# Performance work log

Measured on AMD Instinct MI355X. Metric: run time of the kernel, lower is better.

Reference implementation:

```python
import jax, jax.numpy as jnp
import numpy as np

NUM_PROTOTYPES = 512
NUM_BLOCKS = 8
D_MODEL = 1024
D_BLOCK = D_MODEL // NUM_BLOCKS


def setup_inputs() -> dict:
    key = jax.random.key(0)
    kq, km = jax.random.split(key)
    queries = jax.random.normal(kq, (8, 1024, D_MODEL), dtype=jnp.float32)
    # learned codebook: nn.Embedding(num_blocks*num_prototypes, d_block), normal init
    mem = jax.random.normal(km, (NUM_BLOCKS * NUM_PROTOTYPES, D_BLOCK), dtype=jnp.float32)
    return {"queries": queries, "mem": mem}


def reference(queries, mem):
    B, N, _ = queries.shape
    m, p, d = NUM_BLOCKS, NUM_PROTOTYPES, D_BLOCK
    q = queries.reshape(B, N, m, d)                 # [B,N,m,d]
    codes = mem.reshape(m, p, d)                    # [m,p,d]
    # Squared distances restricted to each query's own block (the only entries
    # the original consumes via distances[i, :, i]):
    #   ||q||^2 - 2 q.c + ||c||^2
    dots = jnp.einsum('bnmd,mpd->bnmp', q, codes)   # [B,N,m,p]
    qn = jnp.sum(q * q, axis=-1)                    # [B,N,m]
    cn = jnp.sum(codes * codes, axis=-1)            # [m,p]
    dist = qn[..., None] - 2.0 * dots + cn[None, None]
    local = jnp.argmin(dist, axis=-1)               # [B,N,m], first-min tiebreak like torch max of -dist
    indices = local + jnp.arange(m, dtype=local.dtype)[None, None, :] * p
    emb = codes[jnp.arange(m)[None, None, :], local]          # [B,N,m,d]
    emb = emb.reshape(B, N, m * d)
    # straight-through estimator
    emb_st = jax.lax.stop_gradient(emb - queries) + queries
    vq_loss = jnp.asarray(0.0, dtype=queries.dtype)
    commitment_loss = jnp.mean((jax.lax.stop_gradient(emb) - queries) ** 2)
    return emb_st, indices, vq_loss, commitment_loss
```

## Files before the change

kernel.cpp:

```cpp
#include <hip/hip_runtime.h>

#define NPROTO 512
#define NBLK 8
#define DB 128
#define DM 1024

#define IDX_OFF  8388608
#define VQ_OFF   8454144
#define CL_OFF   8454145

typedef unsigned short u16;
typedef __attribute__((ext_vector_type(8))) _Float16 f16x8;
typedef __attribute__((ext_vector_type(16))) float f32x16;

#define BH_B   0u
#define BL_B   1048576u
#define CN_B   2097152u
#define PART_B 2113536u
#define WS_NEED (PART_B + 8192u)

__global__ __launch_bounds__(256) void vq_prep(const float* __restrict__ src,
                                               u16* __restrict__ hi,
                                               u16* __restrict__ lo,
                                               float* __restrict__ cn) {
    const int t  = threadIdx.x;
    const int p  = blockIdx.x * 32 + (t >> 3);
    const int g  = t & 7;
    const int m  = p >> 9, pm = p & 511;
    const float* s = src + (size_t)p * DB + g * 16;
    float sq = 0.f;
    ushort4 h[4], l[4];
    #pragma unroll
    for (int j = 0; j < 4; ++j) {
        float4 v = *(const float4*)(s + j * 4);
        float x; _Float16 hf;
        #define S1(c, f) x = v.c; hf = (_Float16)x; h[j].f = __builtin_bit_cast(u16, hf); \
            hf = (_Float16)(x - (float)hf); l[j].f = __builtin_bit_cast(u16, hf); sq += x * x;
        S1(x, x) S1(y, y) S1(z, z) S1(w, w)
        #undef S1
    }
    const size_t o0 = ((size_t)((m * 8 + g) * 2 + 0) * 512 + pm) * 8;
    const size_t o1 = ((size_t)((m * 8 + g) * 2 + 1) * 512 + pm) * 8;
    *(uint4*)(hi + o0) = *(uint4*)&h[0];
    *(uint4*)(hi + o1) = *(uint4*)&h[2];
    *(uint4*)(lo + o0) = *(uint4*)&l[0];
    *(uint4*)(lo + o1) = *(uint4*)&l[2];
    sq += __shfl_xor(sq, 1, 64);
    sq += __shfl_xor(sq, 2, 64);
    sq += __shfl_xor(sq, 4, 64);
    if ((t & 7) == 0) cn[p] = sq;
}

__device__ __forceinline__ unsigned cvt2(float x, float y, unsigned& lo) {
    _Float16 hx = (_Float16)x, hy = (_Float16)y;
    _Float16 lx = (_Float16)(x - (float)hx), ly = (_Float16)(y - (float)hy);
    lo = (unsigned)__builtin_bit_cast(u16, lx) | ((unsigned)__builtin_bit_cast(u16, ly) << 16);
    return (unsigned)__builtin_bit_cast(u16, hx) | ((unsigned)__builtin_bit_cast(u16, hy) << 16);
}

__global__ __launch_bounds__(256, 2) void vq_fused(
        const float* __restrict__ q, const float* __restrict__ mem,
        const u16* __restrict__ bh, const u16* __restrict__ bl,
        const float* __restrict__ cn, float* __restrict__ out,
        float* __restrict__ partials) {
    __shared__ __align__(16) char smem0[16896];
    __shared__ u16  sidxv[4][32][33];
    __shared__ float finalv[4][32];
    __shared__ int   finali[4][32];
    __shared__ float qn_lds[32];
    __shared__ int   bp[32];
    __shared__ float lossbuf[32];

    u16   (*Ap)[8][66][8] = (u16 (*)[8][66][8])smem0;
    float (*sval)[32][33] = (float (*)[32][33])smem0;

    const int t    = threadIdx.x;
    const int lane = t & 63;
    const int w    = t >> 6;
    const int col  = lane & 31;
    const int kg   = lane >> 5;
    const int m    = blockIdx.y;
    const int bn0  = blockIdx.x * 32;

    {
        const int row = t >> 3, g = t & 7;
        const float* src = q + (size_t)(bn0 + row) * DM + m * DB + g * 16;
        float4 v0 = ((const float4*)src)[0];
        float4 v1 = ((const float4*)src)[1];
        float4 v2 = ((const float4*)src)[2];
        float4 v3 = ((const float4*)src)[3];
        float sq = v0.x*v0.x+v0.y*v0.y+v0.z*v0.z+v0.w*v0.w
                 + v1.x*v1.x+v1.y*v1.y+v1.z*v1.z+v1.w*v1.w
                 + v2.x*v2.x+v2.y*v2.y+v2.z*v2.z+v2.w*v2.w
                 + v3.x*v3.x+v3.y*v3.y+v3.z*v3.z+v3.w*v3.w;
        unsigned l0,l1,l2,l3,l4,l5,l6,l7;
        unsigned h0 = cvt2(v0.x, v0.y, l0), h1 = cvt2(v0.z, v0.w, l1);
        unsigned h2 = cvt2(v1.x, v1.y, l2), h3 = cvt2(v1.z, v1.w, l3);
        unsigned h4 = cvt2(v2.x, v2.y, l4), h5 = cvt2(v2.z, v2.w, l5);
        unsigned h6 = cvt2(v3.x, v3.y, l6), h7 = cvt2(v3.z, v3.w, l7);
        *(uint4*)&Ap[0][g][row][0]      = make_uint4(h0, h1, h2, h3);
        *(uint4*)&Ap[0][g][row + 32][0] = make_uint4(h4, h5, h6, h7);
        *(uint4*)&Ap[1][g][row][0]      = make_uint4(l0, l1, l2, l3);
        *(uint4*)&Ap[1][g][row + 32][0] = make_uint4(l4, l5, l6, l7);
        sq += __shfl_xor(sq, 1, 64);
        sq += __shfl_xor(sq, 2, 64);
        sq += __shfl_xor(sq, 4, 64);
        if (g == 0) qn_lds[row] = sq;
    }
    __syncthreads();

    const int pbase = w * 128;
    const u16* bh_l = bh + ((size_t)(m * 16 + kg) * 512 + pbase + col) * 8;
    const u16* bl_l = bl + ((size_t)(m * 16 + kg) * 512 + pbase + col) * 8;

    float bestv[16]; int besti[16];
    #pragma unroll
    for (int r = 0; r < 16; ++r) { bestv[r] = 3.4e38f; besti[r] = 0; }

    #pragma unroll 2
    for (int c = 0; c < 4; ++c) {
        const float cnv = cn[m * NPROTO + pbase + c * 32 + col];
        const u16* bhc = bh_l + c * 256;
        const u16* blc = bl_l + c * 256;
        f32x16 aA, aB;
        #pragma unroll
        for (int r = 0; r < 16; ++r) { aA[r] = 0.f; aB[r] = 0.f; }
        #pragma unroll
        for (int kst = 0; kst < 8; ++kst) {
            f16x8 Bh = *(const f16x8*)(bhc + kst * 8192);
            f16x8 Bl = *(const f16x8*)(blc + kst * 8192);
            f16x8 Ah = *(const f16x8*)&Ap[0][kst][lane][0];
            f16x8 Al = *(const f16x8*)&Ap[1][kst][lane][0];
            aA = __builtin_amdgcn_mfma_f32_32x32x16_f16(Ah, Bh, aA, 0, 0, 0);
            aB = __builtin_amdgcn_mfma_f32_32x32x16_f16(Al, Bh, aB, 0, 0, 0);
            aB = __builtin_amdgcn_mfma_f32_32x32x16_f16(Ah, Bl, aB, 0, 0, 0);
        }
        const int ix = pbase + c * 32 + col;
        #pragma unroll
        for (int r = 0; r < 16; ++r) {
            float d = cnv - 2.0f * (aA[r] + aB[r]);
            if (d < bestv[r]) { bestv[r] = d; besti[r] = ix; }
        }
    }
    __syncthreads();

    #pragma unroll
    for (int r = 0; r < 16; ++r) {
        int row = (r & 3) + 8 * (r >> 2) + 4 * kg;
        sval[w][row][col]  = bestv[r];
        sidxv[w][row][col] = (u16)besti[r];
    }
    __syncthreads();

    {
        const int rrow = col, seg = kg;
        float bv = 3.4e38f; int bi = 0x7fffffff;
        #pragma unroll
        for (int c2 = 0; c2 < 16; ++c2) {
            float v = sval[w][rrow][seg * 16 + c2];
            int  ix = sidxv[w][rrow][seg * 16 + c2];
            if (v < bv || (v == bv && ix < bi)) { bv = v; bi = ix; }
        }
        float v2 = __shfl_xor(bv, 32, 64);
        int   i2 = __shfl_xor(bi, 32, 64);
        if (v2 < bv || (v2 == bv && i2 < bi)) { bv = v2; bi = i2; }
        if (kg == 0) { finalv[w][rrow] = bv; finali[w][rrow] = bi; }
    }
    __syncthreads();

    if (t < 32) {
        float bv = finalv[0][t]; int bi = finali[0][t];
        #pragma unroll
        for (int w2 = 1; w2 < 4; ++w2) {
            float v2 = finalv[w2][t]; int i2 = finali[w2][t];
            if (v2 < bv || (v2 == bv && i2 < bi)) { bv = v2; bi = i2; }
        }
        bp[t] = bi;
        out[(size_t)IDX_OFF + (size_t)(bn0 + t) * NBLK + m] =
            (float)(m * NPROTO + bi);
        lossbuf[t] = bv + qn_lds[t];
    }
    __syncthreads();

    {
        const int row = t >> 3, g = t & 7;
        const float* cv = mem + ((size_t)(m * NPROTO + bp[row])) * DB + g * 16;
        float* ov = out + (size_t)(bn0 + row) * DM + m * DB + g * 16;
        ((float4*)ov)[0] = ((const float4*)cv)[0];
        ((float4*)ov)[1] = ((const float4*)cv)[1];
        ((float4*)ov)[2] = ((const float4*)cv)[2];
        ((float4*)ov)[3] = ((const float4*)cv)[3];
    }
    if (t == 0) {
        float s = 0.f;
        #pragma unroll
        for (int i = 0; i < 32; ++i) s += lossbuf[i];
        partials[blockIdx.y * gridDim.x + blockIdx.x] = s;
    }
}

__global__ __launch_bounds__(256) void vq_init(const float* __restrict__ mem,
                                               float* __restrict__ cn) {
    int p = blockIdx.x * 256 + threadIdx.x;
    const float* c = mem + (size_t)p * DB;
    float s = 0.f;
    #pragma unroll 8
    for (int k = 0; k < DB; k += 4) {
        float4 v = *(const float4*)(c + k);
        s += v.x * v.x + v.y * v.y + v.z * v.z + v.w * v.w;
    }
    cn[p] = s;
}

__global__ __launch_bounds__(256, 1) void vq_main_f32(const float* __restrict__ q,
                                                      const float* __restrict__ mem,
                                                      const float* __restrict__ cn,
                                                      float* __restrict__ out,
                                                      float* __restrict__ partials) {
    __shared__ float q_lds[128 * 132];
    __shared__ float c_lds[128 * 132];
    __shared__ float red[256];

    const int t    = threadIdx.x;
    const int tile = blockIdx.x;
    const int m    = blockIdx.y;
    const int tr   = t >> 4;
    const int tc   = t & 15;
    const int bn0  = tile * 128;

    const float* qbase = q + (size_t)bn0 * DM + m * DB;
    #pragma unroll
    for (int it = 0; it < 16; ++it) {
        int idx = it * 256 + t;
        int row = idx >> 5;
        int c4  = (idx & 31) << 2;
        *(float4*)&q_lds[row * 132 + c4] = *(const float4*)(qbase + (size_t)row * DM + c4);
    }

    float bestv[8]; int besti[8];
    #pragma unroll
    for (int i = 0; i < 8; ++i) { bestv[i] = 3.4e38f; besti[i] = 0; }
    const float* cbase = mem + (size_t)m * NPROTO * DB;

    for (int ch = 0; ch < 4; ++ch) {
        __syncthreads();
        const float* cb = cbase + (size_t)ch * 128 * DB;
        #pragma unroll
        for (int it = 0; it < 16; ++it) {
            int idx = it * 256 + t;
            int row = idx >> 5;
            int c4  = (idx & 31) << 2;
            *(float4*)&c_lds[row * 132 + c4] = *(const float4*)(cb + row * DB + c4);
        }
        __syncthreads();

        float acc[8][8];
        #pragma unroll
        for (int i = 0; i < 8; ++i)
            #pragma unroll
            for (int j = 0; j < 8; ++j) acc[i][j] = 0.f;

        for (int d4 = 0; d4 < DB; d4 += 4) {
            float4 qa[8], cvv[8];
            #pragma unroll
            for (int i = 0; i < 8; ++i) qa[i] = *(const float4*)&q_lds[(tr + 16 * i) * 132 + d4];
            #pragma unroll
            for (int j = 0; j < 8; ++j) cvv[j] = *(const float4*)&c_lds[(tc + 16 * j) * 132 + d4];
            #pragma unroll
            for (int i = 0; i < 8; ++i)
                #pragma unroll
                for (int j = 0; j < 8; ++j) {
                    acc[i][j] += qa[i].x * cvv[j].x; acc[i][j] += qa[i].y * cvv[j].y;
                    acc[i][j] += qa[i].z * cvv[j].z; acc[i][j] += qa[i].w * cvv[j].w;
                }
        }
        #pragma unroll
        for (int i = 0; i < 8; ++i)
            #pragma unroll
            for (int j = 0; j < 8; ++j) {
                int lp = ch * 128 + tc + 16 * j;
                float dist = cn[m * NPROTO + lp] - 2.0f * acc[i][j];
                if (dist < bestv[i]) { bestv[i] = dist; besti[i] = lp; }
            }
    }

    #pragma unroll
    for (int i = 0; i < 8; ++i) {
        float v = bestv[i]; int ix = besti[i];
        #pragma unroll
        for (int off = 1; off < 16; off <<= 1) {
            float v2 = __shfl_xor(v, off, 64);
            int  ix2 = __shfl_xor(ix, off, 64);
            if (v2 < v || (v2 == v && ix2 < ix)) { v = v2; ix = ix2; }
        }
        bestv[i] = v; besti[i] = ix;
    }

    float lacc = 0.f;
    #pragma unroll
    for (int i = 0; i < 8; ++i) {
        int row = tr + 16 * i;
        int bn  = bn0 + row;
        const float* cvec = cbase + (size_t)besti[i] * DB;
        float* orow = out + (size_t)bn * DM + m * DB;
        #pragma unroll
        for (int h = 0; h < 2; ++h) {
            int colx = h * 64 + tc * 4;
            float4 c4v = *(const float4*)(cvec + colx);
            *(float4*)(orow + colx) = c4v;
            float4 qv2 = *(const float4*)&q_lds[row * 132 + colx];
            float dx = c4v.x - qv2.x, dy = c4v.y - qv2.y;
            float dz = c4v.z - qv2.z, dw = c4v.w - qv2.w;
            lacc += dx * dx + dy * dy + dz * dz + dw * dw;
        }
        if (tc == 0)
            out[(size_t)IDX_OFF + (size_t)bn * NBLK + m] = (float)(m * NPROTO + besti[i]);
    }

    red[t] = lacc;
    __syncthreads();
    for (int s = 128; s > 0; s >>= 1) {
        if (t < s) red[t] += red[t + s];
        __syncthreads();
    }
    if (t == 0) partials[blockIdx.y * gridDim.x + blockIdx.x] = red[0];
}

__global__ __launch_bounds__(256) void vq_final(const float* __restrict__ partials,
                                                float* __restrict__ out, int n) {
    __shared__ float red[256];
    int t = threadIdx.x;
    float v = 0.f;
    for (int i = t; i < n; i += 256) v += partials[i];
    red[t] = v;
    __syncthreads();
    for (int s = 128; s > 0; s >>= 1) {
        if (t < s) red[t] += red[t + s];
        __syncthreads();
    }
    if (t == 0) {
        out[VQ_OFF] = 0.f;
        out[CL_OFF] = red[0] / 8388608.0f;
    }
}

extern "C" void kernel_launch(void* const* d_in, const int* in_sizes, int n_in,
                              void* d_out, int out_size, void* d_ws, size_t ws_size,
                              hipStream_t stream) {
    const float* q   = (const float*)d_in[0];
    const float* mem = (const float*)d_in[1];
    float* out = (float*)d_out;
    char* ws = (char*)d_ws;

    if (ws_size >= (size_t)WS_NEED) {
        u16*   bhp = (u16*)(ws + BH_B);
        u16*   blp = (u16*)(ws + BL_B);
        float* cnp = (float*)(ws + CN_B);
        float* partials = (float*)(ws + PART_B);

        vq_prep<<<128, 256, 0, stream>>>(mem, bhp, blp, cnp);
        dim3 grid(256, 8);
        vq_fused<<<grid, 256, 0, stream>>>(q, mem, bhp, blp, cnp, out, partials);
        vq_final<<<1, 256, 0, stream>>>(partials, out, 2048);
    } else {
        float* cn = (float*)ws;
        float* partials = cn + 4096;
        vq_init<<<16, 256, 0, stream>>>(mem, cn);
        dim3 grid(64, 8);
        vq_main_f32<<<grid, 256, 0, stream>>>(q, mem, cn, out, partials);
        vq_final<<<1, 256, 0, stream>>>(partials, out, 512);
    }
}
```

Measured before the change: 72.77 us.

## Give each wave its own query rows and reduce argmin with shuffles

Restructures the fused VQ kernel so each block handles 128 query rows and each wave owns 32 rows over all 512 prototypes. The cross-wave LDS argmin merge and block barriers are removed and replaced by intra-wave shuffle reductions. Per-wave loss partials are written, so the final reduction sums more entries. The trade-off is that each wave now reads the whole codebook slice, which raises B-operand traffic, and the grid becomes smaller with less parallelism.

```diff
diff --git a/kernel.cpp b/kernel.cpp
--- a/kernel.cpp
+++ b/kernel.cpp
@@ -17,7 +17,7 @@
 #define BL_B   1048576u
 #define CN_B   2097152u
 #define PART_B 2113536u
-#define WS_NEED (PART_B + 8192u)
+#define WS_NEED (PART_B + 16384u)
 
 __global__ __launch_bounds__(256) void vq_prep(const float* __restrict__ src,
                                                u16* __restrict__ hi,
@@ -62,17 +62,10 @@
         const float* __restrict__ q, const float* __restrict__ mem,
         const u16* __restrict__ bh, const u16* __restrict__ bl,
         const float* __restrict__ cn, float* __restrict__ out,
-        float* __restrict__ partials) {
-    __shared__ __align__(16) char smem0[16896];
-    __shared__ u16  sidxv[4][32][33];
-    __shared__ float finalv[4][32];
-    __shared__ int   finali[4][32];
-    __shared__ float qn_lds[32];
-    __shared__ int   bp[32];
-    __shared__ float lossbuf[32];
-
-    u16   (*Ap)[8][66][8] = (u16 (*)[8][66][8])smem0;
-    float (*sval)[32][33] = (float (*)[32][33])smem0;
+        float* __restrict__ partials2) {
+    __shared__ __align__(16) u16 Ap[4][2][8][66][8];
+    __shared__ float qn_lds[128];
+    __shared__ int   bp[128];
 
     const int t    = threadIdx.x;
     const int lane = t & 63;
@@ -80,46 +73,49 @@
     const int col  = lane & 31;
     const int kg   = lane >> 5;
     const int m    = blockIdx.y;
-    const int bn0  = blockIdx.x * 32;
+    const int bn0  = blockIdx.x * 128;
+    const int rbase = w * 32;
 
     {
-        const int row = t >> 3, g = t & 7;
-        const float* src = q + (size_t)(bn0 + row) * DM + m * DB + g * 16;
-        float4 v0 = ((const float4*)src)[0];
-        float4 v1 = ((const float4*)src)[1];
-        float4 v2 = ((const float4*)src)[2];
-        float4 v3 = ((const float4*)src)[3];
-        float sq = v0.x*v0.x+v0.y*v0.y+v0.z*v0.z+v0.w*v0.w
-                 + v1.x*v1.x+v1.y*v1.y+v1.z*v1.z+v1.w*v1.w
-                 + v2.x*v2.x+v2.y*v2.y+v2.z*v2.z+v2.w*v2.w
-                 + v3.x*v3.x+v3.y*v3.y+v3.z*v3.z+v3.w*v3.w;
-        unsigned l0,l1,l2,l3,l4,l5,l6,l7;
-        unsigned h0 = cvt2(v0.x, v0.y, l0), h1 = cvt2(v0.z, v0.w, l1);
-        unsigned h2 = cvt2(v1.x, v1.y, l2), h3 = cvt2(v1.z, v1.w, l3);
-        unsigned h4 = cvt2(v2.x, v2.y, l4), h5 = cvt2(v2.z, v2.w, l5);
-        unsigned h6 = cvt2(v3.x, v3.y, l6), h7 = cvt2(v3.z, v3.w, l7);
-        *(uint4*)&Ap[0][g][row][0]      = make_uint4(h0, h1, h2, h3);
-        *(uint4*)&Ap[0][g][row + 32][0] = make_uint4(h4, h5, h6, h7);
-        *(uint4*)&Ap[1][g][row][0]      = make_uint4(l0, l1, l2, l3);
-        *(uint4*)&Ap[1][g][row + 32][0] = make_uint4(l4, l5, l6, l7);
+        const int row = lane >> 1;
+        const int hf  = lane & 1;
+        const float* src = q + (size_t)(bn0 + rbase + row) * DM + m * DB + hf * 64;
+        float sq = 0.f;
+        #pragma unroll
+        for (int k4 = 0; k4 < 4; ++k4) {
+            const int kst = hf * 4 + k4;
+            float4 v0 = ((const float4*)(src + k4 * 16))[0];
+            float4 v1 = ((const float4*)(src + k4 * 16))[1];
+            float4 v2 = ((const float4*)(src + k4 * 16))[2];
+            float4 v3 = ((const float4*)(src + k4 * 16))[3];
+            sq += v0.x*v0.x+v0.y*v0.y+v0.z*v0.z+v0.w*v0.w
+                + v1.x*v1.x+v1.y*v1.y+v1.z*v1.z+v1.w*v1.w
+                + v2.x*v2.x+v2.y*v2.y+v2.z*v2.z+v2.w*v2.w
+                + v3.x*v3.x+v3.y*v3.y+v3.z*v3.z+v3.w*v3.w;
+            unsigned l0,l1,l2,l3,l4,l5,l6,l7;
+            unsigned h0 = cvt2(v0.x, v0.y, l0), h1 = cvt2(v0.z, v0.w, l1);
+            unsigned h2 = cvt2(v1.x, v1.y, l2), h3 = cvt2(v1.z, v1.w, l3);
+            unsigned h4 = cvt2(v2.x, v2.y, l4), h5 = cvt2(v2.z, v2.w, l5);
+            unsigned h6 = cvt2(v3.x, v3.y, l6), h7 = cvt2(v3.z, v3.w, l7);
+            *(uint4*)&Ap[w][0][kst][row][0]      = make_uint4(h0, h1, h2, h3);
+            *(uint4*)&Ap[w][0][kst][row + 32][0] = make_uint4(h4, h5, h6, h7);
+            *(uint4*)&Ap[w][1][kst][row][0]      = make_uint4(l0, l1, l2, l3);
+            *(uint4*)&Ap[w][1][kst][row + 32][0] = make_uint4(l4, l5, l6, l7);
+        }
         sq += __shfl_xor(sq, 1, 64);
-        sq += __shfl_xor(sq, 2, 64);
-        sq += __shfl_xor(sq, 4, 64);
-        if (g == 0) qn_lds[row] = sq;
-    }
-    __syncthreads();
-
-    const int pbase = w * 128;
-    const u16* bh_l = bh + ((size_t)(m * 16 + kg) * 512 + pbase + col) * 8;
-    const u16* bl_l = bl + ((size_t)(m * 16 + kg) * 512 + pbase + col) * 8;
+        if (hf == 0) qn_lds[rbase + row] = sq;
+    }
+
+    const u16* bh_l = bh + ((size_t)(m * 16 + kg) * 512 + col) * 8;
+    const u16* bl_l = bl + ((size_t)(m * 16 + kg) * 512 + col) * 8;
 
     float bestv[16]; int besti[16];
     #pragma unroll
     for (int r = 0; r < 16; ++r) { bestv[r] = 3.4e38f; besti[r] = 0; }
 
     #pragma unroll 2
-    for (int c = 0; c < 4; ++c) {
-        const float cnv = cn[m * NPROTO + pbase + c * 32 + col];
+    for (int c = 0; c < 16; ++c) {
+        const float cnv = cn[m * NPROTO + c * 32 + col];
         const u16* bhc = bh_l + c * 256;
         const u16* blc = bl_l + c * 256;
         f32x16 aA, aB;
@@ -129,73 +125,53 @@
         for (int kst = 0; kst < 8; ++kst) {
             f16x8 Bh = *(const f16x8*)(bhc + kst * 8192);
             f16x8 Bl = *(const f16x8*)(blc + kst * 8192);
-            f16x8 Ah = *(const f16x8*)&Ap[0][kst][lane][0];
-            f16x8 Al = *(const f16x8*)&Ap[1][kst][lane][0];
+            f16x8 Ah = *(const f16x8*)&Ap[w][0][kst][lane][0];
+            f16x8 Al = *(const f16x8*)&Ap[w][1][kst][lane][0];
             aA = __builtin_amdgcn_mfma_f32_32x32x16_f16(Ah, Bh, aA, 0, 0, 0);
             aB = __builtin_amdgcn_mfma_f32_32x32x16_f16(Al, Bh, aB, 0, 0, 0);
             aB = __builtin_amdgcn_mfma_f32_32x32x16_f16(Ah, Bl, aB, 0, 0, 0);
         }
-        const int ix = pbase + c * 32 + col;
+        const int ix = c * 32 + col;
         #pragma unroll
         for (int r = 0; r < 16; ++r) {
             float d = cnv - 2.0f * (aA[r] + aB[r]);
             if (d < bestv[r]) { bestv[r] = d; besti[r] = ix; }
         }
     }
-    __syncthreads();
 
     #pragma unroll
     for (int r = 0; r < 16; ++r) {
-        int row = (r & 3) + 8 * (r >> 2) + 4 * kg;
-        sval[w][row][col]  = bestv[r];
-        sidxv[w][row][col] = (u16)besti[r];
-    }
-    __syncthreads();
+        float v = bestv[r]; int ix = besti[r];
+        #pragma unroll
+        for (int off = 1; off < 32; off <<= 1) {
+            float v2 = __shfl_xor(v, off, 64);
+            int  ix2 = __shfl_xor(ix, off, 64);
+            if (v2 < v || (v2 == v && ix2 < ix)) { v = v2; ix = ix2; }
+        }
+        bestv[r] = v; besti[r] = ix;
+    }
+
+    if (col == 0) {
+        float lp = 0.f;
+        #pragma unroll
+        for (int r = 0; r < 16; ++r) {
+            int row = rbase + (r & 3) + 8 * (r >> 2) + 4 * kg;
+            bp[row] = besti[r];
+            out[(size_t)IDX_OFF + (size_t)(bn0 + row) * NBLK + m] =
+                (float)(m * NPROTO + besti[r]);
+            lp += bestv[r] + qn_lds[row];
+        }
+        partials2[((size_t)blockIdx.y * gridDim.x + blockIdx.x) * 8 + w * 2 + kg] = lp;
+    }
 
     {
-        const int rrow = col, seg = kg;
-        float bv = 3.4e38f; int bi = 0x7fffffff;
-        #pragma unroll
-        for (int c2 = 0; c2 < 16; ++c2) {
-            float v = sval[w][rrow][seg * 16 + c2];
-            int  ix = sidxv[w][rrow][seg * 16 + c2];
-            if (v < bv || (v == bv && ix < bi)) { bv = v; bi = ix; }
-        }
-        float v2 = __shfl_xor(bv, 32, 64);
-        int   i2 = __shfl_xor(bi, 32, 64);
-        if (v2 < bv || (v2 == bv && i2 < bi)) { bv = v2; bi = i2; }
-        if (kg == 0) { finalv[w][rrow] = bv; finali[w][rrow] = bi; }
-    }
-    __syncthreads();
-
-    if (t < 32) {
-        float bv = finalv[0][t]; int bi = finali[0][t];
-        #pragma unroll
-        for (int w2 = 1; w2 < 4; ++w2) {
-            float v2 = finalv[w2][t]; int i2 = finali[w2][t];
-            if (v2 < bv || (v2 == bv && i2 < bi)) { bv = v2; bi = i2; }
-        }
-        bp[t] = bi;
-        out[(size_t)IDX_OFF + (size_t)(bn0 + t) * NBLK + m] =
-            (float)(m * NPROTO + bi);
-        lossbuf[t] = bv + qn_lds[t];
-    }
-    __syncthreads();
-
-    {
-        const int row = t >> 3, g = t & 7;
-        const float* cv = mem + ((size_t)(m * NPROTO + bp[row])) * DB + g * 16;
-        float* ov = out + (size_t)(bn0 + row) * DM + m * DB + g * 16;
-        ((float4*)ov)[0] = ((const float4*)cv)[0];
-        ((float4*)ov)[1] = ((const float4*)cv)[1];
-        ((float4*)ov)[2] = ((const float4*)cv)[2];
-        ((float4*)ov)[3] = ((const float4*)cv)[3];
-    }
-    if (t == 0) {
-        float s = 0.f;
-        #pragma unroll
-        for (int i = 0; i < 32; ++i) s += lossbuf[i];
-        partials[blockIdx.y * gridDim.x + blockIdx.x] = s;
+        const int row = lane >> 1, hf = lane & 1;
+        const int bpi = bp[rbase + row];
+        const float* cv = mem + ((size_t)(m * NPROTO + bpi)) * DB + hf * 64;
+        float* ov = out + (size_t)(bn0 + rbase + row) * DM + m * DB + hf * 64;
+        #pragma unroll
+        for (int j = 0; j < 16; ++j)
+            ((float4*)ov)[j] = ((const float4*)cv)[j];
     }
 }
 
@@ -359,9 +335,9 @@
         float* partials = (float*)(ws + PART_B);
 
         vq_prep<<<128, 256, 0, stream>>>(mem, bhp, blp, cnp);
-        dim3 grid(256, 8);
+        dim3 grid(64, 8);
         vq_fused<<<grid, 256, 0, stream>>>(q, mem, bhp, blp, cnp, out, partials);
-        vq_final<<<1, 256, 0, stream>>>(partials, out, 2048);
+        vq_final<<<1, 256, 0, stream>>>(partials, out, 4096);
     } else {
         float* cn = (float*)ws;
         float* partials = cn + 4096;
```

Result: faster. 69.54 us (-4.4%).
